# Optimization experiments

Hardware: AMD Instinct MI355X
Metric: run time of the kernel (lower is better)

The kernel has to match this reference:

```python
import jax, jax.numpy as jnp
import numpy as np

N, E, H, F = 100000, 1000000, 4, 64
D_IN = 64


def _gat_conv(x, src, dst, W, al, ar, b, act):
    # x: [N, D_in], W: [D_in, H*F], al/ar: [H, F], b: [H, F]
    z = (x @ W).reshape(N, H, F)
    el = jnp.sum(z * al, axis=-1)              # [N, H]
    er = jnp.sum(z * ar, axis=-1)              # [N, H]
    e = jax.nn.leaky_relu(el[src] + er[dst], 0.2)   # [E, H]
    # edge softmax over incoming edges of each dst node
    m = jax.ops.segment_max(e, dst, num_segments=N)  # [N, H]
    ex = jnp.exp(e - m[dst])                         # [E, H]
    s = jax.ops.segment_sum(ex, dst, num_segments=N)  # [N, H]
    alpha = ex / s[dst]                              # [E, H]
    msg = z[src] * alpha[..., None]                  # [E, H, F] (largest intermediate)
    out = jax.ops.segment_sum(msg, dst, num_segments=N) + b  # [N, H, F]
    return act(out)


def setup_inputs() -> dict:
    key = jax.random.key(0)
    ks = jax.random.split(key, 12)
    sc_in = 1.0 / np.sqrt(D_IN)
    sc_f = 1.0 / np.sqrt(F)
    return {
        "x": jax.random.normal(ks[0], (N, D_IN), jnp.float32),
        "src": jax.random.randint(ks[1], (E,), 0, N, jnp.int32),
        "dst": jax.random.randint(ks[2], (E,), 0, N, jnp.int32),
        "W1": jax.random.normal(ks[3], (D_IN, H * F), jnp.float32) * sc_in,
        "al1": jax.random.normal(ks[4], (H, F), jnp.float32) * sc_f,
        "ar1": jax.random.normal(ks[5], (H, F), jnp.float32) * sc_f,
        "b1": jnp.zeros((H, F), jnp.float32),
        "W2": jax.random.normal(ks[6], (F, H * F), jnp.float32) * sc_f,
        "al2": jax.random.normal(ks[7], (H, F), jnp.float32) * sc_f,
        "ar2": jax.random.normal(ks[8], (H, F), jnp.float32) * sc_f,
        "b2": jnp.zeros((H, F), jnp.float32),
    }


def reference(x, src, dst, W1, al1, ar1, b1, W2, al2, ar2, b2):
    # layer 1: GATConv with tanh activation, then mean over heads
    h = _gat_conv(x, src, dst, W1, al1, ar1, b1, jnp.tanh)   # [N, H, F]
    h = h.mean(axis=-2)                                      # [N, F]
    # layer 2: GATConv (no activation), then mean over heads
    h = _gat_conv(h, src, dst, W2, al2, ar2, b2, lambda v: v)
    return h.mean(axis=-2)                                   # [N, F]
```

## Files before the change

kernel.cpp:

```cpp
#include <hip/hip_runtime.h>

typedef _Float16 f16x8 __attribute__((ext_vector_type(8)));
typedef _Float16 f16x4 __attribute__((ext_vector_type(4)));
typedef _Float16 f16x2 __attribute__((ext_vector_type(2)));
typedef float f32x4 __attribute__((ext_vector_type(4)));

#define PADB 16
#define MAXNB 512
#define TILE_A 4096

__device__ __forceinline__ float lrelu(float v) { return v >= 0.f ? v : 0.2f * v; }
__device__ __forceinline__ float cexp(float v) { return __expf(fminf(v, 60.f)); }
__device__ __forceinline__ float ftanh(float x) {
    float e = __expf(fminf(2.f * x, 30.f));
    return (e - 1.f) / (e + 1.f);
}

__global__ __launch_bounds__(256) void k_wprep(
    const float* __restrict__ W1, const float* __restrict__ al1, const float* __restrict__ ar1,
    const float* __restrict__ W2, const float* __restrict__ al2, const float* __restrict__ ar2,
    float* __restrict__ A1l, float* __restrict__ A1r,
    float* __restrict__ A2l, float* __restrict__ A2r,
    _Float16* __restrict__ Wt1, _Float16* __restrict__ Wt2,
    int* __restrict__ bktc, int nb)
{
    int b = blockIdx.x, t = threadIdx.x;
    if (b < 2) {
        const float* W  = b ? W2 : W1;
        const float* al = b ? al2 : al1;
        const float* ar = b ? ar2 : ar1;
        float* Al = b ? A2l : A1l;
        float* Ar = b ? A2r : A1r;
        _Float16* Wt = b ? Wt2 : Wt1;
        int k = t >> 2, h = t & 3;
        float sl = 0.f, sr = 0.f;
#pragma unroll 8
        for (int f = 0; f < 64; ++f) {
            float wv = W[k * 256 + h * 64 + f];
            sl = fmaf(wv, al[h * 64 + f], sl);
            sr = fmaf(wv, ar[h * 64 + f], sr);
        }
        Al[k * 4 + h] = sl;
        Ar[k * 4 + h] = sr;
        int col = t;
#pragma unroll 8
        for (int kk = 0; kk < 64; ++kk)
            Wt[col * 64 + kk] = (_Float16)W[kk * 256 + col];
    } else {
        for (int i = t; i < nb; i += 256) bktc[(size_t)i * PADB] = 0;
    }
}

__global__ __launch_bounds__(256) void k_elr_hist(
    const float* __restrict__ Xf, _Float16* __restrict__ XhOut,
    const float* __restrict__ Al, const float* __restrict__ Ar,
    float* __restrict__ el, float* __restrict__ er, int nNodes,
    const int* __restrict__ dst, int* __restrict__ bktc, int E_, int ebBlocks,
    int nb)
{
    int b = blockIdx.x;
    if (b < ebBlocks) {
        __shared__ int lb[MAXNB];
        int t = threadIdx.x;
        for (int i = t; i < nb; i += 256) lb[i] = 0;
        __syncthreads();
        int base = b * TILE_A;
        int end = base + TILE_A; if (end > E_) end = E_;
        for (int j = base + t; j < end; j += 256)
            atomicAdd(&lb[((unsigned)dst[j]) >> 8], 1);
        __syncthreads();
        for (int i = t; i < nb; i += 256) {
            int c = lb[i];
            if (c) atomicAdd(&bktc[(size_t)i * PADB], c);
        }
        return;
    }
    int lane = threadIdx.x & 63, wid = threadIdx.x >> 6;
    int q = lane >> 4, c = lane & 15;
    int n = (b - ebBlocks) * 16 + wid * 4 + q;
    if (n >= nNodes) return;
    float4 xv = *reinterpret_cast<const float4*>(Xf + (size_t)n * 64 + c * 4);
    f16x4 xh4 = {(_Float16)xv.x, (_Float16)xv.y, (_Float16)xv.z, (_Float16)xv.w};
    *reinterpret_cast<f16x4*>(XhOut + (size_t)n * 64 + c * 4) = xh4;
    float p0 = 0.f, p1 = 0.f, p2 = 0.f, p3 = 0.f;
    float q0 = 0.f, q1 = 0.f, q2 = 0.f, q3 = 0.f;
    float xs[4] = {xv.x, xv.y, xv.z, xv.w};
#pragma unroll
    for (int i = 0; i < 4; ++i) {
        float4 av = *reinterpret_cast<const float4*>(Al + (c * 4 + i) * 4);
        float4 rv = *reinterpret_cast<const float4*>(Ar + (c * 4 + i) * 4);
        p0 = fmaf(xs[i], av.x, p0); p1 = fmaf(xs[i], av.y, p1);
        p2 = fmaf(xs[i], av.z, p2); p3 = fmaf(xs[i], av.w, p3);
        q0 = fmaf(xs[i], rv.x, q0); q1 = fmaf(xs[i], rv.y, q1);
        q2 = fmaf(xs[i], rv.z, q2); q3 = fmaf(xs[i], rv.w, q3);
    }
#pragma unroll
    for (int m = 1; m <= 8; m <<= 1) {
        p0 += __shfl_xor(p0, m, 64); p1 += __shfl_xor(p1, m, 64);
        p2 += __shfl_xor(p2, m, 64); p3 += __shfl_xor(p3, m, 64);
        q0 += __shfl_xor(q0, m, 64); q1 += __shfl_xor(q1, m, 64);
        q2 += __shfl_xor(q2, m, 64); q3 += __shfl_xor(q3, m, 64);
    }
    if (c == 0) {
        *reinterpret_cast<float4*>(el + (size_t)n * 4) = make_float4(p0, p1, p2, p3);
        *reinterpret_cast<float4*>(er + (size_t)n * 4) = make_float4(q0, q1, q2, q3);
    }
}

__global__ __launch_bounds__(256) void k_elr2(
    const _Float16* __restrict__ Xh,
    const float* __restrict__ Al, const float* __restrict__ Ar,
    float* __restrict__ el, float* __restrict__ er, int nNodes)
{
    int lane = threadIdx.x & 63, wid = threadIdx.x >> 6;
    int q = lane >> 4, c = lane & 15;
    int n = blockIdx.x * 16 + wid * 4 + q;
    if (n >= nNodes) return;
    f16x4 xh4 = *reinterpret_cast<const f16x4*>(Xh + (size_t)n * 64 + c * 4);
    float p0 = 0.f, p1 = 0.f, p2 = 0.f, p3 = 0.f;
    float q0 = 0.f, q1 = 0.f, q2 = 0.f, q3 = 0.f;
#pragma unroll
    for (int i = 0; i < 4; ++i) {
        float xs = (float)xh4[i];
        float4 av = *reinterpret_cast<const float4*>(Al + (c * 4 + i) * 4);
        float4 rv = *reinterpret_cast<const float4*>(Ar + (c * 4 + i) * 4);
        p0 = fmaf(xs, av.x, p0); p1 = fmaf(xs, av.y, p1);
        p2 = fmaf(xs, av.z, p2); p3 = fmaf(xs, av.w, p3);
        q0 = fmaf(xs, rv.x, q0); q1 = fmaf(xs, rv.y, q1);
        q2 = fmaf(xs, rv.z, q2); q3 = fmaf(xs, rv.w, q3);
    }
#pragma unroll
    for (int m = 1; m <= 8; m <<= 1) {
        p0 += __shfl_xor(p0, m, 64); p1 += __shfl_xor(p1, m, 64);
        p2 += __shfl_xor(p2, m, 64); p3 += __shfl_xor(p3, m, 64);
        q0 += __shfl_xor(q0, m, 64); q1 += __shfl_xor(q1, m, 64);
        q2 += __shfl_xor(q2, m, 64); q3 += __shfl_xor(q3, m, 64);
    }
    if (c == 0) {
        *reinterpret_cast<float4*>(el + (size_t)n * 4) = make_float4(p0, p1, p2, p3);
        *reinterpret_cast<float4*>(er + (size_t)n * 4) = make_float4(q0, q1, q2, q3);
    }
}

__global__ void k_bscan(const int* __restrict__ bktc, int* __restrict__ bbase,
                        int* __restrict__ bcur, int nb) {
    int lane = threadIdx.x;
    int carry = 0;
    for (int base = 0; base < nb; base += 64) {
        int i = base + lane;
        int v = (i < nb) ? bktc[(size_t)i * PADB] : 0;
        int sc = v;
#pragma unroll
        for (int d = 1; d < 64; d <<= 1) {
            int u = __shfl_up(sc, d, 64);
            if (lane >= d) sc += u;
        }
        if (i < nb) {
            int ex = carry + sc - v;
            bbase[i] = ex;
            bcur[(size_t)i * PADB] = ex;
        }
        carry += __shfl(sc, 63, 64);
    }
    if (lane == 0) bbase[nb] = carry;
}

__global__ __launch_bounds__(256) void k_binA(
    const int* __restrict__ src, const int* __restrict__ dst,
    int* __restrict__ bcur, unsigned* __restrict__ ebkt, int E_, int nb)
{
    __shared__ int lcnt[MAXNB];
    __shared__ int lcur[MAXNB];
    __shared__ int lofs[MAXNB];
    __shared__ int gbase[MAXNB];
    __shared__ unsigned spack[TILE_A];
    __shared__ int gposs[TILE_A];
    int t = threadIdx.x;
    int tile0 = blockIdx.x * TILE_A;
    int cntT = E_ - tile0; if (cntT > TILE_A) cntT = TILE_A;

    for (int i = t; i < nb; i += 256) { lcnt[i] = 0; lcur[i] = 0; }
    __syncthreads();

    int myS[16], myD[16];
#pragma unroll
    for (int k = 0; k < 16; ++k) {
        int idx = k * 256 + t;
        if (idx < cntT) {
            myS[k] = src[tile0 + idx];
            myD[k] = dst[tile0 + idx];
            atomicAdd(&lcnt[((unsigned)myD[k]) >> 8], 1);
        }
    }
    __syncthreads();

    for (int i = t; i < nb; i += 256) {
        int c = lcnt[i];
        gbase[i] = c ? atomicAdd(&bcur[(size_t)i * PADB], c) : 0;
    }
    if (t < 64) {
        int carry = 0;
        for (int base = 0; base < nb; base += 64) {
            int i = base + t;
            int v = (i < nb) ? lcnt[i] : 0;
            int sc = v;
#pragma unroll
            for (int d = 1; d < 64; d <<= 1) {
                int u = __shfl_up(sc, d, 64);
                if (t >= d) sc += u;
            }
            if (i < nb) lofs[i] = carry + sc - v;
            carry += __shfl(sc, 63, 64);
        }
    }
    __syncthreads();

#pragma unroll
    for (int k = 0; k < 16; ++k) {
        int idx = k * 256 + t;
        if (idx < cntT) {
            int b = ((unsigned)myD[k]) >> 8;
            int slot = atomicAdd(&lcur[b], 1);
            int lidx = lofs[b] + slot;
            spack[lidx] = (unsigned)myS[k] | (((unsigned)myD[k] & 255u) << 17);
            gposs[lidx] = gbase[b] + slot;
        }
    }
    __syncthreads();

    for (int j = t; j < cntT; j += 256)
        ebkt[gposs[j]] = spack[j];
}

__global__ __launch_bounds__(256) void k_binC(
    const unsigned* __restrict__ ebkt, const int* __restrict__ bbase,
    int* __restrict__ cnt, int nNodes)
{
    __shared__ int lc[256];
    int b = blockIdx.x, t = threadIdx.x;
    lc[t] = 0;
    __syncthreads();
    int s0 = bbase[b], s1 = bbase[b + 1];
    for (int j = s0 + t; j < s1; j += 256)
        atomicAdd(&lc[ebkt[j] >> 17], 1);
    __syncthreads();
    int node = (b << 8) + t;
    if (node < nNodes) cnt[node] = lc[t];
}

__global__ __launch_bounds__(256) void k_binB(
    const unsigned* __restrict__ ebkt, const int* __restrict__ bbase,
    const int* __restrict__ offs, int* __restrict__ esrc, int nNodes)
{
    __shared__ int lcur[256];
    __shared__ int lofs[256];
    int b = blockIdx.x, t = threadIdx.x;
    lcur[t] = 0;
    int node = (b << 8) + t;
    lofs[t] = (node < nNodes) ? offs[node] : 0;
    __syncthreads();
    int s0 = bbase[b], s1 = bbase[b + 1];
    for (int j = s0 + t; j < s1; j += 256) {
        unsigned v = ebkt[j];
        int dl = v >> 17;
        int p = lofs[dl] + atomicAdd(&lcur[dl], 1);
        esrc[p] = (int)(v & 0x1FFFFu);
    }
}

#define SC_VPT 8
#define SC_CHUNK 2048

__global__ __launch_bounds__(256) void k_chunk_sums(const int* __restrict__ cnt,
                                                    int* __restrict__ bsums, int n) {
    int tid = threadIdx.x;
    int base = blockIdx.x * SC_CHUNK + tid * SC_VPT;
    int s = 0;
#pragma unroll
    for (int i = 0; i < SC_VPT; ++i) { int idx = base + i; if (idx < n) s += cnt[idx]; }
#pragma unroll
    for (int m = 1; m < 64; m <<= 1) s += __shfl_xor(s, m, 64);
    int lane = tid & 63, wid = tid >> 6;
    __shared__ int sh[4];
    if (lane == 0) sh[wid] = s;
    __syncthreads();
    if (tid == 0) bsums[blockIdx.x] = sh[0] + sh[1] + sh[2] + sh[3];
}

__global__ void k_scan_mid(int* bsums, int nb) {
    int lane = threadIdx.x & 63;
    int carry = 0;
    for (int base = 0; base < nb; base += 64) {
        int i = base + lane;
        int v = (i < nb) ? bsums[i] : 0;
        int sc = v;
#pragma unroll
        for (int d = 1; d < 64; d <<= 1) {
            int t = __shfl_up(sc, d, 64);
            if (lane >= d) sc += t;
        }
        if (i < nb) bsums[i] = carry + sc - v;
        carry += __shfl(sc, 63, 64);
    }
}

__global__ __launch_bounds__(256) void k_scan_write(const int* __restrict__ cnt,
                                                    const int* __restrict__ bsums,
                                                    int* __restrict__ offs, int n) {
    int tid = threadIdx.x;
    int base = blockIdx.x * SC_CHUNK + tid * SC_VPT;
    int v[SC_VPT]; int s = 0;
#pragma unroll
    for (int i = 0; i < SC_VPT; ++i) { int idx = base + i; v[i] = (idx < n) ? cnt[idx] : 0; s += v[i]; }
    int lane = tid & 63, wid = tid >> 6;
    int sc = s;
#pragma unroll
    for (int d = 1; d < 64; d <<= 1) { int t = __shfl_up(sc, d, 64); if (lane >= d) sc += t; }
    __shared__ int wsum[4];
    if (lane == 63) wsum[wid] = sc;
    __syncthreads();
    int wbase = 0;
    for (int i = 0; i < wid; ++i) wbase += wsum[i];
    int p = bsums[blockIdx.x] + wbase + (sc - s);
#pragma unroll
    for (int i = 0; i < SC_VPT; ++i) {
        int idx = base + i;
        if (idx < n) {
            offs[idx] = p; p += v[i];
            if (idx == n - 1) offs[n] = p;
        }
    }
}

template <typename OutT>
__global__ __launch_bounds__(256, 4) void k_sgp(
    const int* __restrict__ esrc, const int* __restrict__ offs,
    const float* __restrict__ el, const float* __restrict__ er,
    const _Float16* __restrict__ Xh,
    const _Float16* __restrict__ Wt, const float* __restrict__ B,
    OutT* __restrict__ out, int nNodes, int do_tanh)
{
    __shared__ _Float16 sagg[16 * 264];
    __shared__ int4 sedge[16][17];
    int tid = threadIdx.x;
    int lane = tid & 63, wid = tid >> 6;
    int q = lane >> 4, c = lane & 15, c4 = c * 4;
    int n = blockIdx.x * 16 + wid * 4 + q;
    int nl = wid * 4 + q;
    bool valid = n < nNodes;

    float A0[4] = {}, A1[4] = {}, A2[4] = {}, A3[4] = {};
    if (valid) {
        int s0 = offs[n], s1 = offs[n + 1];
        int d = s1 - s0;
        float4 erv = *reinterpret_cast<const float4*>(er + (size_t)n * 4);

        int sreg = 0;
        float x0 = 0.f, x1 = 0.f, x2 = 0.f, x3 = 0.f;
        if (c < d) {
            sreg = esrc[s0 + c];
            float4 v = *reinterpret_cast<const float4*>(el + (size_t)sreg * 4);
            x0 = cexp(lrelu(v.x + erv.x)); x1 = cexp(lrelu(v.y + erv.y));
            x2 = cexp(lrelu(v.z + erv.z)); x3 = cexp(lrelu(v.w + erv.w));
        }
        float t0 = x0, t1 = x1, t2 = x2, t3 = x3;
        for (int j = s0 + c + 16; j < s1; j += 16) {
            int s = esrc[j];
            float4 v = *reinterpret_cast<const float4*>(el + (size_t)s * 4);
            t0 += cexp(lrelu(v.x + erv.x)); t1 += cexp(lrelu(v.y + erv.y));
            t2 += cexp(lrelu(v.z + erv.z)); t3 += cexp(lrelu(v.w + erv.w));
        }
#pragma unroll
        for (int m = 1; m <= 8; m <<= 1) {
            t0 += __shfl_xor(t0, m, 64); t1 += __shfl_xor(t1, m, 64);
            t2 += __shfl_xor(t2, m, 64); t3 += __shfl_xor(t3, m, 64);
        }
        float i0 = 1.f / t0, i1 = 1.f / t1, i2 = 1.f / t2, i3 = 1.f / t3;

        for (int base = s0; base < s1; base += 16) {
            int cnt_ = s1 - base; if (cnt_ > 16) cnt_ = 16;
            int sj = 0, pk01 = 0, pk23 = 0;
            if (base == s0) {
                if (c < d) {
                    sj = sreg;
                    f16x2 pa = {(_Float16)(x0 * i0), (_Float16)(x1 * i1)};
                    f16x2 pb = {(_Float16)(x2 * i2), (_Float16)(x3 * i3)};
                    pk01 = __builtin_bit_cast(int, pa);
                    pk23 = __builtin_bit_cast(int, pb);
                }
            } else if (c < cnt_) {
                sj = esrc[base + c];
                float4 v = *reinterpret_cast<const float4*>(el + (size_t)sj * 4);
                f16x2 pa = {(_Float16)(cexp(lrelu(v.x + erv.x)) * i0),
                            (_Float16)(cexp(lrelu(v.y + erv.y)) * i1)};
                f16x2 pb = {(_Float16)(cexp(lrelu(v.z + erv.z)) * i2),
                            (_Float16)(cexp(lrelu(v.w + erv.w)) * i3)};
                pk01 = __builtin_bit_cast(int, pa);
                pk23 = __builtin_bit_cast(int, pb);
            }
            sedge[nl][c] = make_int4(sj, pk01, pk23, 0);
            int rnd = (cnt_ + 3) & ~3;
            for (int b = 0; b < rnd; b += 4) {
                int4 ed[4];
                f16x4 xv[4];
#pragma unroll
                for (int u = 0; u < 4; ++u)
                    ed[u] = sedge[nl][b + u];
#pragma unroll
                for (int u = 0; u < 4; ++u)
                    xv[u] = *reinterpret_cast<const f16x4*>(
                        Xh + (size_t)(unsigned)ed[u].x * 64 + c4);
#pragma unroll
                for (int u = 0; u < 4; ++u) {
                    f16x2 wa = __builtin_bit_cast(f16x2, ed[u].y);
                    f16x2 wb = __builtin_bit_cast(f16x2, ed[u].z);
#pragma unroll
                    for (int i = 0; i < 4; ++i) {
                        float xf = (float)xv[u][i];
                        A0[i] = fmaf((float)wa[0], xf, A0[i]);
                        A1[i] = fmaf((float)wa[1], xf, A1[i]);
                        A2[i] = fmaf((float)wb[0], xf, A2[i]);
                        A3[i] = fmaf((float)wb[1], xf, A3[i]);
                    }
                }
            }
        }
    }
    {
        _Float16* aggr = sagg + nl * 264;
        f16x4 h0, h1v, h2, h3;
#pragma unroll
        for (int i = 0; i < 4; ++i) {
            h0[i] = (_Float16)A0[i]; h1v[i] = (_Float16)A1[i];
            h2[i] = (_Float16)A2[i]; h3[i] = (_Float16)A3[i];
        }
        *reinterpret_cast<f16x4*>(aggr + c4)       = h0;
        *reinterpret_cast<f16x4*>(aggr + 64 + c4)  = h1v;
        *reinterpret_cast<f16x4*>(aggr + 128 + c4) = h2;
        *reinterpret_cast<f16x4*>(aggr + 192 + c4) = h3;
    }

    int col = c, quad = q, f0 = wid * 16;
    f16x8 bfrag[4][2];
    float bias[4];
#pragma unroll
    for (int h = 0; h < 4; ++h) {
#pragma unroll
        for (int ks = 0; ks < 2; ++ks)
            bfrag[h][ks] = *reinterpret_cast<const f16x8*>(
                Wt + (h * 64 + f0 + col) * 64 + ks * 32 + quad * 8);
        bias[h] = B[h * 64 + f0 + col];
    }
    __syncthreads();

    const _Float16* ap = sagg + col * 264 + quad * 8;
    f32x4 acc = {0.f, 0.f, 0.f, 0.f};
#pragma unroll
    for (int h = 0; h < 4; ++h) {
        f16x8 a0 = *reinterpret_cast<const f16x8*>(ap + h * 64);
        f16x8 a1 = *reinterpret_cast<const f16x8*>(ap + h * 64 + 32);
        f32x4 dd = {0.f, 0.f, 0.f, 0.f};
        dd = __builtin_amdgcn_mfma_f32_16x16x32_f16(a0, bfrag[h][0], dd, 0, 0, 0);
        dd = __builtin_amdgcn_mfma_f32_16x16x32_f16(a1, bfrag[h][1], dd, 0, 0, 0);
        if (do_tanh) {
#pragma unroll
            for (int r = 0; r < 4; ++r) acc[r] += ftanh(dd[r] + bias[h]);
        } else {
#pragma unroll
            for (int r = 0; r < 4; ++r) acc[r] += dd[r] + bias[h];
        }
    }
    int n0 = blockIdx.x * 16;
#pragma unroll
    for (int r = 0; r < 4; ++r) {
        int row = n0 + quad * 4 + r;
        if (row < nNodes)
            out[(size_t)row * 64 + f0 + col] = (OutT)(0.25f * acc[r]);
    }
}

extern "C" void kernel_launch(void* const* d_in, const int* in_sizes, int n_in,
                              void* d_out, int out_size, void* d_ws, size_t ws_size,
                              hipStream_t stream) {
    const float* x   = (const float*)d_in[0];
    const int*   src = (const int*)d_in[1];
    const int*   dst = (const int*)d_in[2];
    const float* W1  = (const float*)d_in[3];
    const float* al1 = (const float*)d_in[4];
    const float* ar1 = (const float*)d_in[5];
    const float* b1  = (const float*)d_in[6];
    const float* W2  = (const float*)d_in[7];
    const float* al2 = (const float*)d_in[8];
    const float* ar2 = (const float*)d_in[9];
    const float* b2  = (const float*)d_in[10];
    float* out = (float*)d_out;

    int N_ = in_sizes[0] / 64;
    int E_ = in_sizes[1];
    int NB_ = (N_ + 255) >> 8;

    char* ws = (char*)d_ws;
    size_t off = 0;
    auto alloc = [&](size_t bytes) -> void* {
        void* p = ws + off;
        off = (off + bytes + 255) & ~(size_t)255;
        return p;
    };
    _Float16* xh  = (_Float16*)alloc(((size_t)N_ + 16) * 64 * 2);
    _Float16* h1h = (_Float16*)alloc(((size_t)N_ + 16) * 64 * 2);
    float* el   = (float*)alloc(((size_t)N_ + 16) * 4 * 4);
    float* er   = (float*)alloc(((size_t)N_ + 16) * 4 * 4);
    int*   cnt  = (int*)alloc((size_t)(N_ + 16) * 4);
    int*   offs = (int*)alloc((size_t)(N_ + 1) * 4);
    int*   esrc = (int*)alloc((size_t)E_ * 4);
    unsigned* ebkt = (unsigned*)alloc((size_t)E_ * 4);
    int*   bktc = (int*)alloc((size_t)MAXNB * PADB * 4);
    int*   bcur = (int*)alloc((size_t)MAXNB * PADB * 4);
    int*   bbase= (int*)alloc((size_t)(MAXNB + 1) * 4);
    int*   bsums= (int*)alloc(4096);
    float* A1l  = (float*)alloc(64 * 4 * 4);
    float* A1r  = (float*)alloc(64 * 4 * 4);
    float* A2l  = (float*)alloc(64 * 4 * 4);
    float* A2r  = (float*)alloc(64 * 4 * 4);
    _Float16* Wt1 = (_Float16*)alloc(256 * 64 * 2);
    _Float16* Wt2 = (_Float16*)alloc(256 * 64 * 2);

    k_wprep<<<3, 256, 0, stream>>>(W1, al1, ar1, W2, al2, ar2,
                                   A1l, A1r, A2l, A2r, Wt1, Wt2, bktc, NB_);

    int hb = (E_ + TILE_A - 1) / TILE_A;
    int nb16 = (N_ + 15) / 16;
    k_elr_hist<<<hb + nb16, 256, 0, stream>>>(x, xh, A1l, A1r, el, er, N_,
                                              dst, bktc, E_, hb, NB_);
    k_bscan<<<1, 64, 0, stream>>>(bktc, bbase, bcur, NB_);
    k_binA<<<hb, 256, 0, stream>>>(src, dst, bcur, ebkt, E_, NB_);
    k_binC<<<NB_, 256, 0, stream>>>(ebkt, bbase, cnt, N_);
    int nchunks = (N_ + SC_CHUNK - 1) / SC_CHUNK;
    k_chunk_sums<<<nchunks, 256, 0, stream>>>(cnt, bsums, N_);
    k_scan_mid<<<1, 64, 0, stream>>>(bsums, nchunks);
    k_scan_write<<<nchunks, 256, 0, stream>>>(cnt, bsums, offs, N_);
    k_binB<<<NB_, 256, 0, stream>>>(ebkt, bbase, offs, esrc, N_);

    k_sgp<_Float16><<<nb16, 256, 0, stream>>>(esrc, offs, el, er, xh,
                                              Wt1, b1, h1h, N_, 1);
    k_elr2<<<nb16, 256, 0, stream>>>(h1h, A2l, A2r, el, er, N_);
    k_sgp<float><<<nb16, 256, 0, stream>>>(esrc, offs, el, er, h1h,
                                           Wt2, b2, out, N_, 0);
}
```

Measured before the change: 275.7 us.

## Prefetch first-chunk neighbor features before softmax denominator in aggregation kernel

Splits the per-edge shared staging into separate index and alpha arrays so source indices for the first 16 edges can be published before the softmax weights are known. The gathers of neighbour feature rows for the first chunk are issued before the denominator reduction, and then software-pipelined across two register buffers, so gather latency overlaps the exp/shuffle work. Later chunks keep the simple load-then-FMA loop. The prefetch buffers add register pressure under a 4-waves-per-SIMD launch bound, which could cause spills.

```diff
diff --git a/kernel.cpp b/kernel.cpp
--- a/kernel.cpp
+++ b/kernel.cpp
@@ -332,6 +332,24 @@
     }
 }
 
+#define SGP_LOAD(rr, XV) { \
+    _Pragma("unroll") for (int u_ = 0; u_ < 4; ++u_) { \
+        int e_ = sidx[nl][4 * (rr) + u_]; \
+        XV[u_] = *reinterpret_cast<const f16x4*>(Xh + (size_t)(unsigned)e_ * 64 + c4); } }
+
+#define SGP_FMA(rr, XV) { \
+    int2 aw_[4]; \
+    _Pragma("unroll") for (int u_ = 0; u_ < 4; ++u_) aw_[u_] = salp[nl][4 * (rr) + u_]; \
+    _Pragma("unroll") for (int u_ = 0; u_ < 4; ++u_) { \
+        f16x2 wa_ = __builtin_bit_cast(f16x2, aw_[u_].x); \
+        f16x2 wb_ = __builtin_bit_cast(f16x2, aw_[u_].y); \
+        _Pragma("unroll") for (int i_ = 0; i_ < 4; ++i_) { \
+            float xf_ = (float)XV[u_][i_]; \
+            A0[i_] = fmaf((float)wa_[0], xf_, A0[i_]); \
+            A1[i_] = fmaf((float)wa_[1], xf_, A1[i_]); \
+            A2[i_] = fmaf((float)wb_[0], xf_, A2[i_]); \
+            A3[i_] = fmaf((float)wb_[1], xf_, A3[i_]); } } }
+
 template <typename OutT>
 __global__ __launch_bounds__(256, 4) void k_sgp(
     const int* __restrict__ esrc, const int* __restrict__ offs,
@@ -341,7 +359,8 @@
     OutT* __restrict__ out, int nNodes, int do_tanh)
 {
     __shared__ _Float16 sagg[16 * 264];
-    __shared__ int4 sedge[16][17];
+    __shared__ int  sidx[16][17];
+    __shared__ int2 salp[16][17];
     int tid = threadIdx.x;
     int lane = tid & 63, wid = tid >> 6;
     int q = lane >> 4, c = lane & 15, c4 = c * 4;
@@ -353,22 +372,30 @@
     if (valid) {
         int s0 = offs[n], s1 = offs[n + 1];
         int d = s1 - s0;
+        int dc = d > 16 ? 16 : d;
+        int R = (dc + 3) >> 2;
         float4 erv = *reinterpret_cast<const float4*>(er + (size_t)n * 4);
-
-        int sreg = 0;
+        bool has = c < d;
+
+        int sreg = has ? esrc[s0 + c] : 0;
+        sidx[nl][c] = sreg;
+        float4 v = has ? *reinterpret_cast<const float4*>(el + (size_t)sreg * 4)
+                       : make_float4(0.f, 0.f, 0.f, 0.f);
+        f16x4 xva[4], xvb[4];
+        if (R > 0) SGP_LOAD(0, xva);
+        if (R > 1) SGP_LOAD(1, xvb);
+
         float x0 = 0.f, x1 = 0.f, x2 = 0.f, x3 = 0.f;
-        if (c < d) {
-            sreg = esrc[s0 + c];
-            float4 v = *reinterpret_cast<const float4*>(el + (size_t)sreg * 4);
+        if (has) {
             x0 = cexp(lrelu(v.x + erv.x)); x1 = cexp(lrelu(v.y + erv.y));
             x2 = cexp(lrelu(v.z + erv.z)); x3 = cexp(lrelu(v.w + erv.w));
         }
         float t0 = x0, t1 = x1, t2 = x2, t3 = x3;
         for (int j = s0 + c + 16; j < s1; j += 16) {
             int s = esrc[j];
-            float4 v = *reinterpret_cast<const float4*>(el + (size_t)s * 4);
-            t0 += cexp(lrelu(v.x + erv.x)); t1 += cexp(lrelu(v.y + erv.y));
-            t2 += cexp(lrelu(v.z + erv.z)); t3 += cexp(lrelu(v.w + erv.w));
+            float4 w = *reinterpret_cast<const float4*>(el + (size_t)s * 4);
+            t0 += cexp(lrelu(w.x + erv.x)); t1 += cexp(lrelu(w.y + erv.y));
+            t2 += cexp(lrelu(w.z + erv.z)); t3 += cexp(lrelu(w.w + erv.w));
         }
 #pragma unroll
         for (int m = 1; m <= 8; m <<= 1) {
@@ -377,52 +404,40 @@
         }
         float i0 = 1.f / t0, i1 = 1.f / t1, i2 = 1.f / t2, i3 = 1.f / t3;
 
-        for (int base = s0; base < s1; base += 16) {
+        int2 ap = make_int2(0, 0);
+        if (has) {
+            f16x2 pa = {(_Float16)(x0 * i0), (_Float16)(x1 * i1)};
+            f16x2 pb = {(_Float16)(x2 * i2), (_Float16)(x3 * i3)};
+            ap.x = __builtin_bit_cast(int, pa);
+            ap.y = __builtin_bit_cast(int, pb);
+        }
+        salp[nl][c] = ap;
+
+        if (R > 0) { SGP_FMA(0, xva); if (R > 2) SGP_LOAD(2, xva); }
+        if (R > 1) { SGP_FMA(1, xvb); if (R > 3) SGP_LOAD(3, xvb); }
+        if (R > 2) SGP_FMA(2, xva);
+        if (R > 3) SGP_FMA(3, xvb);
+
+        for (int base = s0 + 16; base < s1; base += 16) {
             int cnt_ = s1 - base; if (cnt_ > 16) cnt_ = 16;
-            int sj = 0, pk01 = 0, pk23 = 0;
-            if (base == s0) {
-                if (c < d) {
-                    sj = sreg;
-                    f16x2 pa = {(_Float16)(x0 * i0), (_Float16)(x1 * i1)};
-                    f16x2 pb = {(_Float16)(x2 * i2), (_Float16)(x3 * i3)};
-                    pk01 = __builtin_bit_cast(int, pa);
-                    pk23 = __builtin_bit_cast(int, pb);
-                }
-            } else if (c < cnt_) {
+            int sj = 0; int2 a2 = make_int2(0, 0);
+            if (c < cnt_) {
                 sj = esrc[base + c];
-                float4 v = *reinterpret_cast<const float4*>(el + (size_t)sj * 4);
-                f16x2 pa = {(_Float16)(cexp(lrelu(v.x + erv.x)) * i0),
-                            (_Float16)(cexp(lrelu(v.y + erv.y)) * i1)};
-                f16x2 pb = {(_Float16)(cexp(lrelu(v.z + erv.z)) * i2),
-                            (_Float16)(cexp(lrelu(v.w + erv.w)) * i3)};
-                pk01 = __builtin_bit_cast(int, pa);
-                pk23 = __builtin_bit_cast(int, pb);
+                float4 w = *reinterpret_cast<const float4*>(el + (size_t)sj * 4);
+                f16x2 pa = {(_Float16)(cexp(lrelu(w.x + erv.x)) * i0),
+                            (_Float16)(cexp(lrelu(w.y + erv.y)) * i1)};
+                f16x2 pb = {(_Float16)(cexp(lrelu(w.z + erv.z)) * i2),
+                            (_Float16)(cexp(lrelu(w.w + erv.w)) * i3)};
+                a2.x = __builtin_bit_cast(int, pa);
+                a2.y = __builtin_bit_cast(int, pb);
             }
-            sedge[nl][c] = make_int4(sj, pk01, pk23, 0);
-            int rnd = (cnt_ + 3) & ~3;
-            for (int b = 0; b < rnd; b += 4) {
-                int4 ed[4];
-                f16x4 xv[4];
-#pragma unroll
-                for (int u = 0; u < 4; ++u)
-                    ed[u] = sedge[nl][b + u];
-#pragma unroll
-                for (int u = 0; u < 4; ++u)
-                    xv[u] = *reinterpret_cast<const f16x4*>(
-                        Xh + (size_t)(unsigned)ed[u].x * 64 + c4);
-#pragma unroll
-                for (int u = 0; u < 4; ++u) {
-                    f16x2 wa = __builtin_bit_cast(f16x2, ed[u].y);
-                    f16x2 wb = __builtin_bit_cast(f16x2, ed[u].z);
-#pragma unroll
-                    for (int i = 0; i < 4; ++i) {
-                        float xf = (float)xv[u][i];
-                        A0[i] = fmaf((float)wa[0], xf, A0[i]);
-                        A1[i] = fmaf((float)wa[1], xf, A1[i]);
-                        A2[i] = fmaf((float)wb[0], xf, A2[i]);
-                        A3[i] = fmaf((float)wb[1], xf, A3[i]);
-                    }
-                }
+            sidx[nl][c] = sj;
+            salp[nl][c] = a2;
+            int rnd = (cnt_ + 3) >> 2;
+            for (int r = 0; r < rnd; ++r) {
+                f16x4 xr[4];
+                SGP_LOAD(r, xr);
+                SGP_FMA(r, xr);
             }
         }
     }
```

After: 274.5 us. Within noise of the previous version (-0.4%).
